# Optimization experiments

Hardware: AMD Instinct MI355X
Metric: run time of the kernel (lower is better)

Reference implementation:

```python
import jax, jax.numpy as jnp
import numpy as np

# Complex-YOLO / YOLOv2 anchors (anchor_step = 2)
ANCHORS = np.array([1.08, 1.19, 3.42, 4.41, 6.63, 11.38, 9.42, 5.11, 16.62, 10.52], np.float32).reshape(5, 2)
NA = 5          # num_anchors
NC = 8          # num_classes
COORD_SCALE = 1.0
NOOBJECT_SCALE = 1.0
OBJECT_SCALE = 10.0
CLASS_SCALE = 1.0
SIL_THRESH = 0.6

B, H, W, T = 32, 32, 64, 50


def setup_inputs() -> dict:
    key = jax.random.key(0)
    k1, k2 = jax.random.split(key)
    output = jax.random.normal(k1, (B, NA * (7 + NC), H, W), dtype=jnp.float32)
    # target layout: (cls, x, y, w, l, im, re), normalized coords in (0,1); col 1 != 0 => valid box
    target = jax.random.uniform(k2, (B, T, 7), dtype=jnp.float32, minval=0.01, maxval=1.0)
    return {"output": output, "target": target}


def _iou_cxcywh(b1, b2):
    # b1, b2: (..., 4) as (cx, cy, w, h); axis-aligned IoU, matching bbox_ious(x1y1x2y2=False)
    mx = jnp.minimum(b1[..., 0] - b1[..., 2] / 2, b2[..., 0] - b2[..., 2] / 2)
    Mx = jnp.maximum(b1[..., 0] + b1[..., 2] / 2, b2[..., 0] + b2[..., 2] / 2)
    my = jnp.minimum(b1[..., 1] - b1[..., 3] / 2, b2[..., 1] - b2[..., 3] / 2)
    My = jnp.maximum(b1[..., 1] + b1[..., 3] / 2, b2[..., 1] + b2[..., 3] / 2)
    cw = b1[..., 2] + b2[..., 2] - (Mx - mx)
    ch = b1[..., 3] + b2[..., 3] - (My - my)
    inter = jnp.where((cw > 0) & (ch > 0), cw * ch, 0.0)
    union = b1[..., 2] * b1[..., 3] + b2[..., 2] * b2[..., 3] - inter
    return inter / union


def _region_loss(output, target):
    nB, _, nH, nW = output.shape
    anc = jnp.asarray(ANCHORS)  # [NA, 2]
    out = output.reshape(nB, NA, 7 + NC, nH, nW)
    x = jax.nn.sigmoid(out[:, :, 0])
    y = jax.nn.sigmoid(out[:, :, 1])
    w = out[:, :, 2]
    l = out[:, :, 3]
    im = out[:, :, 4]
    re = out[:, :, 5]
    conf = jax.nn.sigmoid(out[:, :, 6])
    cls_logits = jnp.moveaxis(out[:, :, 7:], 2, -1)  # [B, A, H, W, C]

    # ---- decoded pred boxes (detached, like .data in torch) ----
    sg = jax.lax.stop_gradient
    grid_x = jnp.arange(nW, dtype=jnp.float32)
    grid_y = jnp.arange(nH, dtype=jnp.float32)
    pbx = sg(x) + grid_x[None, None, None, :]
    pby = sg(y) + grid_y[None, None, :, None]
    pbw = jnp.exp(sg(w)) * anc[None, :, 0, None, None]
    pbl = jnp.exp(sg(l)) * anc[None, :, 1, None, None]
    pred = jnp.stack([pbx, pby, pbw, pbl], axis=-1).reshape(nB, NA * nH * nW, 4)  # [B, N, 4]

    # ---- build_targets (fully vectorized) ----
    tgt = sg(target)
    nT = tgt.shape[1]
    valid = jnp.cumprod((tgt[..., 1] != 0).astype(jnp.int32), axis=1).astype(bool)  # break-on-zero semantics
    gx = tgt[..., 1] * nW
    gy = tgt[..., 2] * nH
    gw = tgt[..., 3] * nW
    gl = tgt[..., 4] * nH
    gi = jnp.clip(gx.astype(jnp.int32), 0, nW - 1)
    gj = jnp.clip(gy.astype(jnp.int32), 0, nH - 1)
    gt = jnp.stack([gx, gy, gw, gl], axis=-1)  # [B, T, 4]

    # IoU of every pred box against every GT -> silence mask
    ious = _iou_cxcywh(gt[:, :, None, :], pred[:, None, :, :])  # [B, T, N]
    ious = jnp.where(valid[..., None], ious, 0.0)
    max_iou = ious.max(axis=1)  # [B, N]
    conf_mask = jnp.where(max_iou > SIL_THRESH, 0.0, NOOBJECT_SCALE).reshape(nB, NA, nH, nW)

    # anchor matching: IoU of (0,0,gw,gl) vs (0,0,aw,ah) -> closed form
    inter_a = jnp.minimum(gw[..., None], anc[None, None, :, 0]) * jnp.minimum(gl[..., None], anc[None, None, :, 1])
    union_a = (gw * gl)[..., None] + (anc[:, 0] * anc[:, 1])[None, None, :] - inter_a
    a_iou = inter_a / union_a  # [B, T, A]
    best_n = jnp.argmax(a_iou, axis=-1)
    aw = anc[best_n, 0]
    al = anc[best_n, 1]

    # winner cell per GT; later GTs overwrite earlier ones at the same cell (torch loop order)
    b_idx = jnp.arange(nB)[:, None]
    lin = ((b_idx * NA + best_n) * nH + gj) * nW + gi  # [B, T]
    M = nB * NA * nH * nW
    t_eff = jnp.where(valid, jnp.arange(nT)[None, :], -1)
    seg = jax.ops.segment_max(t_eff.reshape(-1), lin.reshape(-1), num_segments=M)
    keep = valid & (t_eff == seg[lin])
    lin_safe = jnp.where(keep, lin, M).reshape(-1)  # route losers to dummy slot

    def scat(vals):
        return jnp.zeros(M + 1, jnp.float32).at[lin_safe].set(vals.reshape(-1))[:M].reshape(nB, NA, nH, nW)

    cm = scat(keep.astype(jnp.float32))           # coord_mask == cls_mask
    tx = scat(gx - gi)
    ty = scat(gy - gj)
    tw = scat(jnp.log(gw / aw))
    tl = scat(jnp.log(gl / al))
    tim = scat(tgt[..., 5])
    tre = scat(tgt[..., 6])
    tcls = scat(tgt[..., 0]).astype(jnp.int32)

    n_idx = best_n * (nH * nW) + gj * nW + gi
    pb = pred[b_idx, n_idx]                       # [B, T, 4] pred box at winner cell
    tconf = scat(_iou_cxcywh(gt, pb))
    conf_mask = jnp.where(cm > 0, OBJECT_SCALE, conf_mask)

    # ---- masked losses ----
    def mse(p, t):
        return jnp.sum((p * cm - t * cm) ** 2)

    loss_x = COORD_SCALE * mse(x, tx)
    loss_y = COORD_SCALE * mse(y, ty)
    loss_w = COORD_SCALE * mse(w, tw)
    loss_l = COORD_SCALE * mse(l, tl)
    loss_im = COORD_SCALE * mse(im, tim)
    loss_re = COORD_SCALE * mse(re, tre)
    loss_conf = jnp.sum((conf * conf_mask - tconf * conf_mask) ** 2)
    ce = jax.nn.logsumexp(cls_logits, axis=-1) - jnp.take_along_axis(cls_logits, tcls[..., None], axis=-1)[..., 0]
    loss_cls = CLASS_SCALE * jnp.sum(cm * ce)
    return loss_x + loss_y + loss_w + loss_l + loss_conf + loss_cls + loss_im + loss_re


def reference(output, target):
    return _region_loss(output, target)
```

## Files before the change

### kernel.cpp

```cpp
#include <hip/hip_runtime.h>
#include <math.h>

#define NB 32
#define NA 5
#define NC 8
#define NH 32
#define NW 64
#define NT 50
#define NCH (7 + NC)
#define HW (NH * NW)
#define M_CELLS (NB * NA * NH * NW)
#define OBJECT_SCALE 10.0f
#define SIL_THRESH 0.6f

__constant__ float c_anchors[NA * 2] = {
    1.08f, 1.19f, 3.42f, 4.41f, 6.63f, 11.38f, 9.42f, 5.11f, 16.62f, 10.52f};

__device__ __forceinline__ float sigmoidf(float v) {
    return 1.0f / (1.0f + expf(-v));
}

__device__ __forceinline__ float iou_cxcywh(float ax, float ay, float aw, float ah,
                                            float bx, float by, float bw, float bh) {
    float mx = fminf(ax - aw * 0.5f, bx - bw * 0.5f);
    float Mx = fmaxf(ax + aw * 0.5f, bx + bw * 0.5f);
    float my = fminf(ay - ah * 0.5f, by - bh * 0.5f);
    float My = fmaxf(ay + ah * 0.5f, by + bh * 0.5f);
    float cw = aw + bw - (Mx - mx);
    float ch = ah + bh - (My - my);
    float inter = (cw > 0.0f && ch > 0.0f) ? cw * ch : 0.0f;
    float uni = aw * ah + bw * bh - inter;
    return inter / uni;
}

__global__ void init_kernel(int* __restrict__ tidx, float* __restrict__ out, int out_size) {
    int idx = blockIdx.x * blockDim.x + threadIdx.x;
    if (idx < M_CELLS) tidx[idx] = -1;
    if (idx < out_size) out[idx] = 0.0f;
}

__global__ void target_kernel(const float* __restrict__ target,
                              int* __restrict__ tidx,
                              float* __restrict__ tinfo) {
    int b = blockIdx.x;
    int t = threadIdx.x;
    if (t >= NT) return;
    const float* tp = target + (b * NT + t) * 7;

    bool valid = true;
    for (int tt = 0; tt <= t; ++tt) {
        if (target[(b * NT + tt) * 7 + 1] == 0.0f) { valid = false; break; }
    }

    float gx = tp[1] * (float)NW;
    float gy = tp[2] * (float)NH;
    float gw = tp[3] * (float)NW;
    float gl = tp[4] * (float)NH;

    float* ti = tinfo + (b * NT + t) * 8;
    ti[0] = gx; ti[1] = gy; ti[2] = gw; ti[3] = gl;
    ti[4] = tp[0]; ti[5] = tp[5]; ti[6] = tp[6];
    ti[7] = valid ? 1.0f : 0.0f;
    if (!valid) return;

    int best_n = 0;
    float best = -1.0f;
    for (int a = 0; a < NA; ++a) {
        float aw = c_anchors[2 * a], al = c_anchors[2 * a + 1];
        float inter = fminf(gw, aw) * fminf(gl, al);
        float uni = gw * gl + aw * al - inter;
        float iou = inter / uni;
        if (iou > best) { best = iou; best_n = a; }
    }

    int gi = min(max((int)gx, 0), NW - 1);
    int gj = min(max((int)gy, 0), NH - 1);
    int lin = ((b * NA + best_n) * NH + gj) * NW + gi;
    atomicMax(&tidx[lin], t);
}

__global__ __launch_bounds__(256) void cell_kernel(const float* __restrict__ output,
                                                   const float* __restrict__ tinfo,
                                                   const int* __restrict__ tidx,
                                                   float* __restrict__ out) {
    const int blocks_per_b = (NA * HW) / 256;
    int b = blockIdx.x / blocks_per_b;
    int m_local = (blockIdx.x % blocks_per_b) * 256 + threadIdx.x;
    int a = m_local / HW;
    int rem = m_local - a * HW;
    int j = rem / NW;
    int i = rem - j * NW;

    __shared__ float s_t[NT][8];
    for (int idx = threadIdx.x; idx < NT * 8; idx += 256)
        ((float*)s_t)[idx] = tinfo[b * NT * 8 + idx];
    __syncthreads();

    const float* op = output + ((size_t)(b * NA + a) * NCH) * HW + j * NW + i;
    float o[NCH];
#pragma unroll
    for (int c = 0; c < NCH; ++c) o[c] = op[(size_t)c * HW];

    float x = sigmoidf(o[0]);
    float y = sigmoidf(o[1]);
    float w = o[2], l = o[3], im = o[4], re = o[5];
    float conf = sigmoidf(o[6]);

    float aw = c_anchors[2 * a], al = c_anchors[2 * a + 1];
    float pbx = x + (float)i;
    float pby = y + (float)j;
    float pbw = expf(w) * aw;
    float pbl = expf(l) * al;

    float max_iou = 0.0f;
    for (int t = 0; t < NT; ++t) {
        if (s_t[t][7] == 0.0f) break;
        float iou = iou_cxcywh(s_t[t][0], s_t[t][1], s_t[t][2], s_t[t][3],
                               pbx, pby, pbw, pbl);
        max_iou = fmaxf(max_iou, iou);
    }

    float conf_mask = (max_iou > SIL_THRESH) ? 0.0f : 1.0f;
    float loss = 0.0f;
    float tconf = 0.0f;

    int t = tidx[((b * NA + a) * NH + j) * NW + i];
    if (t >= 0) {
        float gx = s_t[t][0], gy = s_t[t][1], gw = s_t[t][2], gl = s_t[t][3];
        float tx = gx - (float)i;
        float ty = gy - (float)j;
        float tw = logf(gw / aw);
        float tl = logf(gl / al);
        float tim = s_t[t][5], tre = s_t[t][6];
        tconf = iou_cxcywh(gx, gy, gw, gl, pbx, pby, pbw, pbl);
        conf_mask = OBJECT_SCALE;

        float dx = x - tx, dy = y - ty, dw = w - tw, dl = l - tl;
        float di = im - tim, dr = re - trunc(0.0f) * 0.0f - tre;
        dr = re - tre;
        loss += dx * dx + dy * dy + dw * dw + dl * dl + di * di + dr * dr;

        int tcls = (int)s_t[t][4];
        tcls = min(max(tcls, 0), NC - 1);
        float mx = o[7];
#pragma unroll
        for (int c = 1; c < NC; ++c) mx = fmaxf(mx, o[7 + c]);
        float s = 0.0f;
#pragma unroll
        for (int c = 0; c < NC; ++c) s += expf(o[7 + c] - mx);
        loss += (mx + logf(s)) - o[7 + tcls];
    }

    float d = conf * conf_mask - tconf * conf_mask;
    loss += d * d;

    for (int off = 32; off > 0; off >>= 1)
        loss += __shfl_down(loss, off, 64);
    __shared__ float s_part[4];
    int wave = threadIdx.x >> 6;
    int lane = threadIdx.x & 63;
    if (lane == 0) s_part[wave] = loss;
    __syncthreads();
    if (threadIdx.x == 0) {
        atomicAdd(out, s_part[0] + s_part[1] + s_part[2] + s_part[3]);
    }
}

extern "C" void kernel_launch(void* const* d_in, const int* in_sizes, int n_in,
                              void* d_out, int out_size, void* d_ws, size_t ws_size,
                              hipStream_t stream) {
    const float* output = (const float*)d_in[0];
    const float* target = (const float*)d_in[1];
    float* out = (float*)d_out;
    int* tidx = (int*)d_ws;
    float* tinfo = (float*)((char*)d_ws + (size_t)M_CELLS * sizeof(int));

    hipLaunchKernelGGL(init_kernel, dim3((M_CELLS + 255) / 256), dim3(256), 0, stream,
                       tidx, out, out_size);
    hipLaunchKernelGGL(target_kernel, dim3(NB), dim3(64), 0, stream,
                       target, tidx, tinfo);
    hipLaunchKernelGGL(cell_kernel, dim3(NB * 40), dim3(256), 0, stream,
                       output, tinfo, tidx, out);
}
```

Baseline: 101.5 us.

## Drop cell index map, precompute target boxes, and test IoU threshold without division

Removes the init kernel and the per-cell target-index array. Each cell now finds its assigned target by comparing an encoded (anchor, row, col) code while looping over the valid targets. The prep kernel computes the valid count with a ballot and stores precomputed box edges, areas and regression targets. The IoU threshold test becomes inter - 0.6*union > 0, so the loop has no division, and the shared-memory staging becomes direct global (cached) reads. Duplicate-cell assignment now takes the last target by loop order, which matches the old atomicMax semantics, and storing the code as a float is exact for these sizes.

```diff
diff --git a/kernel.cpp b/kernel.cpp
--- a/kernel.cpp
+++ b/kernel.cpp
@@ -9,9 +9,7 @@
 #define NT 50
 #define NCH (7 + NC)
 #define HW (NH * NW)
-#define M_CELLS (NB * NA * NH * NW)
 #define OBJECT_SCALE 10.0f
-#define SIL_THRESH 0.6f
 
 __constant__ float c_anchors[NA * 2] = {
     1.08f, 1.19f, 3.42f, 4.41f, 6.63f, 11.38f, 9.42f, 5.11f, 16.62f, 10.52f};
@@ -20,51 +18,35 @@
     return 1.0f / (1.0f + expf(-v));
 }
 
-__device__ __forceinline__ float iou_cxcywh(float ax, float ay, float aw, float ah,
-                                            float bx, float by, float bw, float bh) {
-    float mx = fminf(ax - aw * 0.5f, bx - bw * 0.5f);
-    float Mx = fmaxf(ax + aw * 0.5f, bx + bw * 0.5f);
-    float my = fminf(ay - ah * 0.5f, by - bh * 0.5f);
-    float My = fmaxf(ay + ah * 0.5f, by + bh * 0.5f);
-    float cw = aw + bw - (Mx - mx);
-    float ch = ah + bh - (My - my);
-    float inter = (cw > 0.0f && ch > 0.0f) ? cw * ch : 0.0f;
-    float uni = aw * ah + bw * bh - inter;
-    return inter / uni;
-}
-
-__global__ void init_kernel(int* __restrict__ tidx, float* __restrict__ out, int out_size) {
-    int idx = blockIdx.x * blockDim.x + threadIdx.x;
-    if (idx < M_CELLS) tidx[idx] = -1;
-    if (idx < out_size) out[idx] = 0.0f;
-}
-
-__global__ void target_kernel(const float* __restrict__ target,
-                              int* __restrict__ tidx,
-                              float* __restrict__ tinfo) {
+__global__ void prep_kernel(const float* __restrict__ target,
+                            int* __restrict__ nvalid,
+                            float* __restrict__ tinfo,
+                            float* __restrict__ out) {
     int b = blockIdx.x;
     int t = threadIdx.x;
+    const float* tp = target + (size_t)(b * NT + t) * 7;
+
+    float t0 = 0.f, t1 = 0.f, t2 = 0.f, t3 = 0.f, t4 = 0.f, t5 = 0.f, t6 = 0.f;
+    if (t < NT) {
+        t0 = tp[0]; t1 = tp[1]; t2 = tp[2]; t3 = tp[3];
+        t4 = tp[4]; t5 = tp[5]; t6 = tp[6];
+    }
+    unsigned long long bal = __ballot(t < NT && t1 != 0.0f);
+    if (t == 0) {
+        int nv = __ffsll((unsigned long long)~bal) - 1;
+        nvalid[b] = nv;
+        if (b == 0) out[0] = 0.0f;
+    }
     if (t >= NT) return;
-    const float* tp = target + (b * NT + t) * 7;
 
-    bool valid = true;
-    for (int tt = 0; tt <= t; ++tt) {
-        if (target[(b * NT + tt) * 7 + 1] == 0.0f) { valid = false; break; }
-    }
-
-    float gx = tp[1] * (float)NW;
-    float gy = tp[2] * (float)NH;
-    float gw = tp[3] * (float)NW;
-    float gl = tp[4] * (float)NH;
-
-    float* ti = tinfo + (b * NT + t) * 8;
-    ti[0] = gx; ti[1] = gy; ti[2] = gw; ti[3] = gl;
-    ti[4] = tp[0]; ti[5] = tp[5]; ti[6] = tp[6];
-    ti[7] = valid ? 1.0f : 0.0f;
-    if (!valid) return;
+    float gx = t1 * (float)NW;
+    float gy = t2 * (float)NH;
+    float gw = t3 * (float)NW;
+    float gl = t4 * (float)NH;
 
     int best_n = 0;
     float best = -1.0f;
+#pragma unroll
     for (int a = 0; a < NA; ++a) {
         float aw = c_anchors[2 * a], al = c_anchors[2 * a + 1];
         float inter = fminf(gw, aw) * fminf(gl, al);
@@ -72,87 +54,121 @@
         float iou = inter / uni;
         if (iou > best) { best = iou; best_n = a; }
     }
+    float aw = c_anchors[2 * best_n], al = c_anchors[2 * best_n + 1];
 
     int gi = min(max((int)gx, 0), NW - 1);
     int gj = min(max((int)gy, 0), NH - 1);
-    int lin = ((b * NA + best_n) * NH + gj) * NW + gi;
-    atomicMax(&tidx[lin], t);
+
+    float* ti = tinfo + (size_t)(b * NT + t) * 16;
+    ti[0] = gx - gw * 0.5f;
+    ti[1] = gx + gw * 0.5f;
+    ti[2] = gy - gl * 0.5f;
+    ti[3] = gy + gl * 0.5f;
+    ti[4] = gw;
+    ti[5] = gl;
+    ti[6] = gw * gl;
+    ti[7] = (float)((best_n << 12) | (gj << 6) | gi);
+    ti[8] = gx - (float)gi;
+    ti[9] = gy - (float)gj;
+    ti[10] = t5;
+    ti[11] = t6;
+    ti[12] = t0;
+    ti[13] = logf(gw / aw);
+    ti[14] = logf(gl / al);
+    ti[15] = 0.f;
 }
 
 __global__ __launch_bounds__(256) void cell_kernel(const float* __restrict__ output,
                                                    const float* __restrict__ tinfo,
-                                                   const int* __restrict__ tidx,
+                                                   const int* __restrict__ nvalid,
                                                    float* __restrict__ out) {
     const int blocks_per_b = (NA * HW) / 256;
     int b = blockIdx.x / blocks_per_b;
-    int m_local = (blockIdx.x % blocks_per_b) * 256 + threadIdx.x;
-    int a = m_local / HW;
-    int rem = m_local - a * HW;
-    int j = rem / NW;
-    int i = rem - j * NW;
+    int m = (blockIdx.x % blocks_per_b) * 256 + threadIdx.x;
+    int a = m >> 11;
+    int rem = m & (HW - 1);
+    int j = rem >> 6;
+    int i = rem & (NW - 1);
 
-    __shared__ float s_t[NT][8];
-    for (int idx = threadIdx.x; idx < NT * 8; idx += 256)
-        ((float*)s_t)[idx] = tinfo[b * NT * 8 + idx];
-    __syncthreads();
-
-    const float* op = output + ((size_t)(b * NA + a) * NCH) * HW + j * NW + i;
+    const float* op = output + (size_t)(b * NA + a) * NCH * HW + (j << 6) + i;
     float o[NCH];
 #pragma unroll
     for (int c = 0; c < NCH; ++c) o[c] = op[(size_t)c * HW];
 
     float x = sigmoidf(o[0]);
     float y = sigmoidf(o[1]);
-    float w = o[2], l = o[3], im = o[4], re = o[5];
     float conf = sigmoidf(o[6]);
 
     float aw = c_anchors[2 * a], al = c_anchors[2 * a + 1];
     float pbx = x + (float)i;
     float pby = y + (float)j;
-    float pbw = expf(w) * aw;
-    float pbl = expf(l) * al;
+    float pbw = expf(o[2]) * aw;
+    float pbl = expf(o[3]) * al;
 
-    float max_iou = 0.0f;
-    for (int t = 0; t < NT; ++t) {
-        if (s_t[t][7] == 0.0f) break;
-        float iou = iou_cxcywh(s_t[t][0], s_t[t][1], s_t[t][2], s_t[t][3],
-                               pbx, pby, pbw, pbl);
-        max_iou = fmaxf(max_iou, iou);
+    float plx = pbx - pbw * 0.5f;
+    float phx = pbx + pbw * 0.5f;
+    float ply = pby - pbl * 0.5f;
+    float phy = pby + pbl * 0.5f;
+    float parea = pbw * pbl;
+    float mycode = (float)((a << 12) | (j << 6) | i);
+
+    int nv = nvalid[b];
+    const float* tb = tinfo + (size_t)b * NT * 16;
+
+    float silm = -1.0f;
+    int ta = -1;
+    for (int t = 0; t < nv; ++t) {
+        const float* ti = tb + t * 16;
+        float tlx = ti[0], thx = ti[1], tly = ti[2], thy = ti[3];
+        float gw = ti[4], gl = ti[5], tarea = ti[6], code = ti[7];
+        float mx = fminf(tlx, plx);
+        float Mx = fmaxf(thx, phx);
+        float my = fminf(tly, ply);
+        float My = fmaxf(thy, phy);
+        float cw = (gw + pbw) - (Mx - mx);
+        float ch = (gl + pbl) - (My - my);
+        float inter = (cw > 0.0f && ch > 0.0f) ? cw * ch : 0.0f;
+        float uni = tarea + parea - inter;
+        silm = fmaxf(silm, inter - 0.6f * uni);
+        if (code == mycode) ta = t;
     }
 
-    float conf_mask = (max_iou > SIL_THRESH) ? 0.0f : 1.0f;
-    float loss = 0.0f;
-    float tconf = 0.0f;
+    float loss;
+    if (ta >= 0) {
+        const float* ti = tb + (size_t)ta * 16;
+        float tlx = ti[0], thx = ti[1], tly = ti[2], thy = ti[3];
+        float gw = ti[4], gl = ti[5], tarea = ti[6];
+        float mx = fminf(tlx, plx);
+        float Mx = fmaxf(thx, phx);
+        float my = fminf(tly, ply);
+        float My = fmaxf(thy, phy);
+        float cw = (gw + pbw) - (Mx - mx);
+        float ch = (gl + pbl) - (My - my);
+        float inter = (cw > 0.0f && ch > 0.0f) ? cw * ch : 0.0f;
+        float tconf = inter / (tarea + parea - inter);
 
-    int t = tidx[((b * NA + a) * NH + j) * NW + i];
-    if (t >= 0) {
-        float gx = s_t[t][0], gy = s_t[t][1], gw = s_t[t][2], gl = s_t[t][3];
-        float tx = gx - (float)i;
-        float ty = gy - (float)j;
-        float tw = logf(gw / aw);
-        float tl = logf(gl / al);
-        float tim = s_t[t][5], tre = s_t[t][6];
-        tconf = iou_cxcywh(gx, gy, gw, gl, pbx, pby, pbw, pbl);
-        conf_mask = OBJECT_SCALE;
+        float dx = x - ti[8];
+        float dy = y - ti[9];
+        float dw = o[2] - ti[13];
+        float dl = o[3] - ti[14];
+        float di = o[4] - ti[10];
+        float dr = o[5] - ti[11];
+        loss = dx * dx + dy * dy + dw * dw + dl * dl + di * di + dr * dr;
 
-        float dx = x - tx, dy = y - ty, dw = w - tw, dl = l - tl;
-        float di = im - tim, dr = re - trunc(0.0f) * 0.0f - tre;
-        dr = re - tre;
-        loss += dx * dx + dy * dy + dw * dw + dl * dl + di * di + dr * dr;
+        float dc = OBJECT_SCALE * (conf - tconf);
+        loss += dc * dc;
 
-        int tcls = (int)s_t[t][4];
-        tcls = min(max(tcls, 0), NC - 1);
-        float mx = o[7];
+        int tcls = min(max((int)ti[12], 0), NC - 1);
+        float mxl = o[7];
 #pragma unroll
-        for (int c = 1; c < NC; ++c) mx = fmaxf(mx, o[7 + c]);
+        for (int c = 1; c < NC; ++c) mxl = fmaxf(mxl, o[7 + c]);
         float s = 0.0f;
 #pragma unroll
-        for (int c = 0; c < NC; ++c) s += expf(o[7 + c] - mx);
-        loss += (mx + logf(s)) - o[7 + tcls];
+        for (int c = 0; c < NC; ++c) s += expf(o[7 + c] - mxl);
+        loss += (mxl + logf(s)) - o[7 + tcls];
+    } else {
+        loss = (silm > 0.0f) ? 0.0f : conf * conf;
     }
-
-    float d = conf * conf_mask - tconf * conf_mask;
-    loss += d * d;
 
     for (int off = 32; off > 0; off >>= 1)
         loss += __shfl_down(loss, off, 64);
@@ -161,9 +177,8 @@
     int lane = threadIdx.x & 63;
     if (lane == 0) s_part[wave] = loss;
     __syncthreads();
-    if (threadIdx.x == 0) {
+    if (threadIdx.x == 0)
         atomicAdd(out, s_part[0] + s_part[1] + s_part[2] + s_part[3]);
-    }
 }
 
 extern "C" void kernel_launch(void* const* d_in, const int* in_sizes, int n_in,
@@ -172,13 +187,11 @@
     const float* output = (const float*)d_in[0];
     const float* target = (const float*)d_in[1];
     float* out = (float*)d_out;
-    int* tidx = (int*)d_ws;
-    float* tinfo = (float*)((char*)d_ws + (size_t)M_CELLS * sizeof(int));
+    int* nvalid = (int*)d_ws;
+    float* tinfo = (float*)((char*)d_ws + 128);
 
-    hipLaunchKernelGGL(init_kernel, dim3((M_CELLS + 255) / 256), dim3(256), 0, stream,
-                       tidx, out, out_size);
-    hipLaunchKernelGGL(target_kernel, dim3(NB), dim3(64), 0, stream,
-                       target, tidx, tinfo);
+    hipLaunchKernelGGL(prep_kernel, dim3(NB), dim3(64), 0, stream,
+                       target, nvalid, tinfo, out);
     hipLaunchKernelGGL(cell_kernel, dim3(NB * 40), dim3(256), 0, stream,
-                       output, tinfo, tidx, out);
+                       output, tinfo, nvalid, out);
 }
```

After: 95.08 us. -6.3%, faster.
